# Kernel optimization log

Hardware: AMD Instinct MI355X
Metric: run time of the kernel (lower is better)

The kernel has to match this reference:

```python
import jax, jax.numpy as jnp
import numpy as np

NUM_HEADS = 8
ALPHA = 4.0
BN_EPS = 1e-5


def _dwconv(x, w, pad):
    # x: [B, C, H, W], w: [C, 1, kh, kw] depthwise (groups == C)
    return jax.lax.conv_general_dilated(
        x, w, window_strides=(1, 1), padding=[(pad, pad), (pad, pad)],
        dimension_numbers=('NCHW', 'OIHW', 'NCHW'),
        feature_group_count=x.shape[1])


def _forward(x, qg_w, kv_w, proj_w, proj_b, dwc_w, dwc_b, power_p, scale_p,
             enh_w, bn_gamma, bn_beta, enhance_weight, pos_enc):
    B, N, C = x.shape
    H = W = int(round(N ** 0.5))
    h = NUM_HEADS
    d = C // h

    # qg linear (no bias): [B, N, 2C] -> q, g
    qg = jnp.einsum('bnc,oc->bno', x, qg_w)
    q, g = qg[..., :C], qg[..., C:]

    # SpatialFilterEnhancer on q: depthwise 3x3 conv + BN(train) + ReLU
    qi = q.transpose(0, 2, 1).reshape(B, C, H, W)
    qe = _dwconv(qi, enh_w, pad=1)
    m = qe.mean(axis=(0, 2, 3), keepdims=True)
    var = qe.var(axis=(0, 2, 3), keepdims=True)
    qe = (qe - m) * jax.lax.rsqrt(var + BN_EPS)
    qe = qe * bn_gamma[None, :, None, None] + bn_beta[None, :, None, None]
    qe = jax.nn.relu(qe)
    q_enh = qe.reshape(B, C, N).transpose(0, 2, 1)
    q = q + enhance_weight * q_enh

    # kv linear (sr_ratio == 1 path)
    kv = jnp.einsum('bnc,oc->bno', x, kv_w)
    k, v = kv[..., :C], kv[..., C:]
    k = k + pos_enc  # learned positional encoding, shape [1, N, C]
    n = k.shape[1]

    scale = jax.nn.softplus(scale_p)              # [1, 1, C]
    power = 1.0 + ALPHA * jax.nn.sigmoid(power_p)  # [1, h, 1, d]
    q = q / scale
    k = k / scale

    # split heads: [B, h, N, d]
    q = q.reshape(B, N, h, d).transpose(0, 2, 1, 3)
    k = k.reshape(B, n, h, d).transpose(0, 2, 1, 3)
    v = v.reshape(B, n, h, d).transpose(0, 2, 1, 3)

    # power-law kernel feature maps
    q_pos = jax.nn.relu(q) ** power
    q_neg = jax.nn.relu(-q) ** power
    k_pos = jax.nn.relu(k) ** power
    k_neg = jax.nn.relu(-k) ** power
    q_sim = jnp.concatenate([q_pos, q_neg], axis=-1)   # [B, h, N, 2d]
    q_opp = jnp.concatenate([q_neg, q_pos], axis=-1)
    kf = jnp.concatenate([k_pos, k_neg], axis=-1)      # [B, h, n, 2d]
    v1, v2 = jnp.split(v, 2, axis=-1)                  # [B, h, n, d/2] each

    k_mean = kf.mean(axis=-2)  # [B, h, 2d]
    inv_n = 1.0 / n

    # sim branch
    z = 1.0 / (jnp.einsum('bhnd,bhd->bhn', q_sim, k_mean)[..., None] + 1e-6)
    kv1 = jnp.einsum('bhnd,bhne->bhde', kf, v1) * inv_n  # (n^-0.5)*(n^-0.5)
    x_sim = jnp.einsum('bhnd,bhde->bhne', q_sim, kv1) * z

    # opp branch
    z2 = 1.0 / (jnp.einsum('bhnd,bhd->bhn', q_opp, k_mean)[..., None] + 1e-6)
    kv2 = jnp.einsum('bhnd,bhne->bhde', kf, v2) * inv_n
    x_opp = jnp.einsum('bhnd,bhde->bhne', q_opp, kv2) * z2

    xa = jnp.concatenate([x_sim, x_opp], axis=-1)       # [B, h, N, d]
    xa = xa.transpose(0, 2, 1, 3).reshape(B, N, C)

    # depthwise conv positional branch on v (sr_ratio == 1 -> no interpolate)
    vimg = v.reshape(B * h, H, W, d).transpose(0, 3, 1, 2)  # [B*h, d, H, W]
    vd = _dwconv(vimg, dwc_w, pad=2) + dwc_b[None, :, None, None]
    v_out = vd.reshape(B, C, N).transpose(0, 2, 1)          # [B, N, C]

    out = (xa + v_out) * g
    out = jnp.einsum('bnc,oc->bno', out, proj_w) + proj_b
    return out


def setup_inputs() -> dict:
    key = jax.random.key(0)
    ks = jax.random.split(key, 10)
    B, N, C = 8, 3136, 512
    h = NUM_HEADS
    d = C // h
    f = lambda k, shape, s=0.02: jax.random.normal(k, shape, jnp.float32) * s
    return dict(
        x=jax.random.normal(ks[0], (B, N, C), jnp.float32),
        qg_w=f(ks[1], (2 * C, C)),
        kv_w=f(ks[2], (2 * C, C)),
        proj_w=f(ks[3], (C, C)),
        proj_b=jnp.zeros((C,), jnp.float32),
        dwc_w=f(ks[4], (d, 1, 5, 5), 0.1),
        dwc_b=jnp.zeros((d,), jnp.float32),
        power_p=f(ks[5], (1, h, 1, d), 0.1),
        scale_p=f(ks[6], (1, 1, C), 0.1),
        enh_w=f(ks[7], (C, 1, 3, 3), 0.1),
        bn_gamma=jnp.ones((C,), jnp.float32),
        bn_beta=jnp.zeros((C,), jnp.float32),
        enhance_weight=jnp.float32(0.5),
        pos_enc=f(ks[8], (1, N, C)),
    )


def reference(x, qg_w, kv_w, proj_w, proj_b, dwc_w, dwc_b, power_p, scale_p,
              enh_w, bn_gamma, bn_beta, enhance_weight, pos_enc):
    return _forward(x, qg_w, kv_w, proj_w, proj_b, dwc_w, dwc_b, power_p,
                    scale_p, enh_w, bn_gamma, bn_beta, enhance_weight, pos_enc)
```

## Files before the change

kernel.cpp:

```cpp
#include <hip/hip_runtime.h>
#include <hip/hip_bf16.h>
#include <math.h>

#define CDIM 512
#define NTOK 3136
#define BATCH 8
#define MTOT (BATCH*NTOK)
#define NHEAD 8
#define DHEAD 64
#define HW 56

typedef __attribute__((ext_vector_type(8))) short short8;
typedef __attribute__((ext_vector_type(4))) float f32x4;

__device__ __forceinline__ ushort f2bf(float f) {
    union { float f; unsigned int u; } v; v.f = f;
    unsigned int u = v.u + 0x7FFFu + ((v.u >> 16) & 1u);
    return (ushort)(u >> 16);
}
__device__ __forceinline__ float bf2f(ushort u) {
    union { unsigned int u; float f; } v; v.u = ((unsigned int)u) << 16;
    return v.f;
}

__device__ __forceinline__ void gload_lds16(const void* g, void* lds) {
    __builtin_amdgcn_global_load_lds((const __attribute__((address_space(1))) void*)g,
                                     (__attribute__((address_space(3))) void*)lds,
                                     16, 0, 0);
}

__global__ void prep_kernel(const float* __restrict__ scale_p,
                            const float* __restrict__ power_p,
                            float* __restrict__ inv_scale,
                            float* __restrict__ power) {
    int c = threadIdx.x;
    if (c < CDIM) {
        float s = log1pf(expf(scale_p[c]));
        inv_scale[c] = 1.0f / s;
        power[c] = 1.0f + 4.0f / (1.0f + expf(-power_p[c]));
    }
}

__global__ __launch_bounds__(256) void cvt_bf16_kernel(const float* __restrict__ src,
                                                       ushort* __restrict__ dst, int n4) {
    int i = blockIdx.x * 256 + threadIdx.x;
    if (i < n4) {
        float4 f = ((const float4*)src)[i];
        ushort4 o;
        o.x = f2bf(f.x); o.y = f2bf(f.y); o.z = f2bf(f.z); o.w = f2bf(f.w);
        ((ushort4*)dst)[i] = o;
    }
}

__global__ __launch_bounds__(256) void mgemm_qgkv(const ushort* __restrict__ A,
                                                  const ushort* __restrict__ Wqg,
                                                  const ushort* __restrict__ Wkv,
                                                  ushort* __restrict__ Qout,
                                                  ushort* __restrict__ Gout,
                                                  ushort* __restrict__ KFout,
                                                  ushort* __restrict__ Vout,
                                                  const float* __restrict__ pos,
                                                  const float* __restrict__ invs,
                                                  const float* __restrict__ powr) {
    __shared__ __align__(16) char smem[32768];
    ushort* At = (ushort*)smem;
    ushort* Bt = (ushort*)(smem + 16384);
    float*  Osh = (float*)smem;

    const int t = threadIdx.x;
    const int w = t >> 6, l = t & 63;
    const int wr = w >> 1, wc = w & 1;

    const int bid = blockIdx.x;
    const int idp = (bid & 7) * 392 + (bid >> 3);
    const int mb = idp >> 4, ob = idp & 15;
    const int m0 = mb * 128;
    const ushort* Bp = (ob < 8) ? (Wqg + (size_t)ob * 128 * CDIM)
                                : (Wkv + (size_t)(ob - 8) * 128 * CDIM);

    auto stage = [&](int buf, int ks) {
        const int k0 = ks * 32;
        #pragma unroll
        for (int i = 0; i < 2; ++i) {
            int f = t + i * 256;
            int r = f >> 2, ps = f & 3;
            int ls = ps ^ ((r >> 2) & 3);
            gload_lds16(A + (size_t)(m0 + r) * CDIM + k0 + ls * 8, At + buf * 4096 + f * 8);
            gload_lds16(Bp + (size_t)r * CDIM + k0 + ls * 8, Bt + buf * 4096 + f * 8);
        }
    };

    f32x4 acc[4][4] = {};
    const int psl = (l >> 4) ^ ((l >> 2) & 3);
    stage(0, 0);
    __syncthreads();
    for (int ks = 0; ks < 16; ++ks) {
        int cur = ks & 1;
        if (ks < 15) stage(cur ^ 1, ks + 1);
        short8 af[4], bfr[4];
        #pragma unroll
        for (int i = 0; i < 4; ++i) {
            int row = wr * 64 + i * 16 + (l & 15);
            af[i] = *(const short8*)&At[cur * 4096 + row * 32 + psl * 8];
            int rowb = wc * 64 + i * 16 + (l & 15);
            bfr[i] = *(const short8*)&Bt[cur * 4096 + rowb * 32 + psl * 8];
        }
        #pragma unroll
        for (int i = 0; i < 4; ++i)
            #pragma unroll
            for (int j = 0; j < 4; ++j)
                acc[i][j] = __builtin_amdgcn_mfma_f32_16x16x32_bf16(af[i], bfr[j], acc[i][j], 0, 0, 0);
        __syncthreads();
    }

    const int colbase = ob * 128;
    #pragma unroll
    for (int p = 0; p < 2; ++p) {
        if (wr == p) {
            #pragma unroll
            for (int i = 0; i < 4; ++i)
                #pragma unroll
                for (int j = 0; j < 4; ++j)
                    #pragma unroll
                    for (int rr = 0; rr < 4; ++rr) {
                        int r = i * 16 + (l >> 4) * 4 + rr;
                        int c = wc * 64 + j * 16 + (l & 15);
                        int pc = (c + ((r & 4) << 2)) & 127;
                        Osh[r * 128 + pc] = acc[i][j][rr];
                    }
        }
        __syncthreads();
        #pragma unroll
        for (int q = 0; q < 8; ++q) {
            int fi = q * 256 + t;
            int rl = fi >> 5;
            int r = p * 64 + rl;
            int c4 = (fi & 31) * 4;
            int pc = (c4 + ((rl & 4) << 2)) & 127;
            float4 v = *(float4*)&Osh[rl * 128 + pc];
            int m = m0 + r;
            if (colbase < 512) {
                ushort4 o;
                o.x = f2bf(v.x); o.y = f2bf(v.y); o.z = f2bf(v.z); o.w = f2bf(v.w);
                *(ushort4*)&Qout[(size_t)m * CDIM + colbase + c4] = o;
            } else if (colbase < 1024) {
                ushort4 o;
                o.x = f2bf(v.x); o.y = f2bf(v.y); o.z = f2bf(v.z); o.w = f2bf(v.w);
                *(ushort4*)&Gout[(size_t)m * CDIM + colbase - 512 + c4] = o;
            } else if (colbase < 1536) {
                int n = m % NTOK;
                int oc = colbase - 1024 + c4;
                float4 pv = *(const float4*)&pos[(size_t)n * CDIM + oc];
                float4 iv = *(const float4*)&invs[oc];
                float4 pw = *(const float4*)&powr[oc];
                float kx0 = (v.x + pv.x) * iv.x, kx1 = (v.y + pv.y) * iv.y;
                float kx2 = (v.z + pv.z) * iv.z, kx3 = (v.w + pv.w) * iv.w;
                float t0 = __powf(fabsf(kx0), pw.x), t1 = __powf(fabsf(kx1), pw.y);
                float t2 = __powf(fabsf(kx2), pw.z), t3 = __powf(fabsf(kx3), pw.w);
                ushort4 up, un;
                up.x = kx0 > 0.f ? f2bf(t0) : 0; un.x = kx0 < 0.f ? f2bf(t0) : 0;
                up.y = kx1 > 0.f ? f2bf(t1) : 0; un.y = kx1 < 0.f ? f2bf(t1) : 0;
                up.z = kx2 > 0.f ? f2bf(t2) : 0; un.z = kx2 < 0.f ? f2bf(t2) : 0;
                up.w = kx3 > 0.f ? f2bf(t3) : 0; un.w = kx3 < 0.f ? f2bf(t3) : 0;
                ushort* dst = KFout + (size_t)m * 1024 + ((oc >> 6) << 7) + (oc & 63);
                *(ushort4*)dst = up;
                *(ushort4*)(dst + 64) = un;
            } else {
                ushort4 o;
                o.x = f2bf(v.x); o.y = f2bf(v.y); o.z = f2bf(v.z); o.w = f2bf(v.w);
                *(ushort4*)&Vout[(size_t)m * CDIM + colbase - 1536 + c4] = o;
            }
        }
        __syncthreads();
    }
}

__global__ __launch_bounds__(256) void mgemm_proj(const ushort* __restrict__ A,
                                                  const ushort* __restrict__ W,
                                                  float* __restrict__ out,
                                                  const float* __restrict__ pb) {
    __shared__ __align__(16) char smem[32768];
    ushort* At = (ushort*)smem;
    ushort* Bt = (ushort*)(smem + 16384);
    float*  Osh = (float*)smem;

    const int t = threadIdx.x;
    const int w = t >> 6, l = t & 63;
    const int wr = w >> 1, wc = w & 1;

    const int bid = blockIdx.x;
    const int idp = (bid & 7) * 98 + (bid >> 3);
    const int mb = idp >> 2, ob = idp & 3;
    const int m0 = mb * 128;
    const ushort* Bp = W + (size_t)ob * 128 * CDIM;

    auto stage = [&](int buf, int ks) {
        const int k0 = ks * 32;
        #pragma unroll
        for (int i = 0; i < 2; ++i) {
            int f = t + i * 256;
            int r = f >> 2, ps = f & 3;
            int ls = ps ^ ((r >> 2) & 3);
            gload_lds16(A + (size_t)(m0 + r) * CDIM + k0 + ls * 8, At + buf * 4096 + f * 8);
            gload_lds16(Bp + (size_t)r * CDIM + k0 + ls * 8, Bt + buf * 4096 + f * 8);
        }
    };

    f32x4 acc[4][4] = {};
    const int psl = (l >> 4) ^ ((l >> 2) & 3);
    stage(0, 0);
    __syncthreads();
    for (int ks = 0; ks < 16; ++ks) {
        int cur = ks & 1;
        if (ks < 15) stage(cur ^ 1, ks + 1);
        short8 af[4], bfr[4];
        #pragma unroll
        for (int i = 0; i < 4; ++i) {
            int row = wr * 64 + i * 16 + (l & 15);
            af[i] = *(const short8*)&At[cur * 4096 + row * 32 + psl * 8];
            int rowb = wc * 64 + i * 16 + (l & 15);
            bfr[i] = *(const short8*)&Bt[cur * 4096 + rowb * 32 + psl * 8];
        }
        #pragma unroll
        for (int i = 0; i < 4; ++i)
            #pragma unroll
            for (int j = 0; j < 4; ++j)
                acc[i][j] = __builtin_amdgcn_mfma_f32_16x16x32_bf16(af[i], bfr[j], acc[i][j], 0, 0, 0);
        __syncthreads();
    }

    const int colbase = ob * 128;
    #pragma unroll
    for (int p = 0; p < 2; ++p) {
        if (wr == p) {
            #pragma unroll
            for (int i = 0; i < 4; ++i)
                #pragma unroll
                for (int j = 0; j < 4; ++j)
                    #pragma unroll
                    for (int rr = 0; rr < 4; ++rr) {
                        int r = i * 16 + (l >> 4) * 4 + rr;
                        int c = wc * 64 + j * 16 + (l & 15);
                        int pc = (c + ((r & 4) << 2)) & 127;
                        Osh[r * 128 + pc] = acc[i][j][rr];
                    }
        }
        __syncthreads();
        #pragma unroll
        for (int q = 0; q < 8; ++q) {
            int fi = q * 256 + t;
            int rl = fi >> 5;
            int r = p * 64 + rl;
            int c4 = (fi & 31) * 4;
            int pc = (c4 + ((rl & 4) << 2)) & 127;
            float4 v = *(float4*)&Osh[rl * 128 + pc];
            float4 b4 = *(const float4*)&pb[colbase + c4];
            v.x += b4.x; v.y += b4.y; v.z += b4.z; v.w += b4.w;
            *(float4*)&out[(size_t)(m0 + r) * CDIM + colbase + c4] = v;
        }
        __syncthreads();
    }
}

__global__ __launch_bounds__(256) void conv3s_kernel(const ushort* __restrict__ Qbf,
                                                     const float* __restrict__ enh_w,
                                                     ushort* __restrict__ QEbf,
                                                     float* __restrict__ ssum,
                                                     float* __restrict__ ssq) {
    const int t = threadIdx.x;
    const int c0 = t * 2;
    const int xpos = blockIdx.x;
    const int byc = blockIdx.y;
    const int b = byc >> 2, yc = byc & 3;
    const int y0 = yc * 14;

    float wgt[9][2];
    #pragma unroll
    for (int tap = 0; tap < 9; ++tap) {
        wgt[tap][0] = enh_w[c0 * 9 + tap];
        wgt[tap][1] = enh_w[(c0 + 1) * 9 + tap];
    }
    const size_t base = (size_t)b * NTOK * CDIM + c0;

    float2 win[3][3];
    auto ldrow = [&](int yy, float2* dst) {
        #pragma unroll
        for (int dx = 0; dx < 3; ++dx) {
            int xx = xpos + dx - 1;
            bool ok = (yy >= 0 && yy < HW && xx >= 0 && xx < HW);
            if (ok) {
                ushort2 uv = *(const ushort2*)(Qbf + base + ((size_t)(yy * HW + xx) << 9));
                dst[dx] = make_float2(bf2f(uv.x), bf2f(uv.y));
            } else {
                dst[dx] = make_float2(0.f, 0.f);
            }
        }
    };
    ldrow(y0 - 1, win[0]);
    ldrow(y0,     win[1]);

    float s1a = 0.f, s2a = 0.f, s1b = 0.f, s2b = 0.f;
    #pragma unroll
    for (int i = 0; i < 14; ++i) {
        int y = y0 + i;
        ldrow(y + 1, win[(i + 2) % 3]);
        float a0 = 0.f, a1 = 0.f;
        #pragma unroll
        for (int dy = 0; dy < 3; ++dy) {
            float2* row = win[(i + dy) % 3];
            #pragma unroll
            for (int dx = 0; dx < 3; ++dx) {
                a0 = fmaf(row[dx].x, wgt[dy * 3 + dx][0], a0);
                a1 = fmaf(row[dx].y, wgt[dy * 3 + dx][1], a1);
            }
        }
        ushort2 o; o.x = f2bf(a0); o.y = f2bf(a1);
        *(ushort2*)(QEbf + base + ((size_t)(y * HW + xpos) << 9)) = o;
        s1a += a0; s2a += a0 * a0;
        s1b += a1; s2b += a1 * a1;
    }
    atomicAdd(&ssum[c0], s1a);     atomicAdd(&ssq[c0], s2a);
    atomicAdd(&ssum[c0 + 1], s1b); atomicAdd(&ssq[c0 + 1], s2b);
}

__global__ void bnprep_kernel(const float* __restrict__ ssum, const float* __restrict__ ssq,
                              const float* __restrict__ bn_g, const float* __restrict__ bn_b,
                              float* __restrict__ achan, float* __restrict__ bchan) {
    int c = threadIdx.x;
    if (c < CDIM) {
        const float invM = 1.0f / (float)MTOT;
        float mean = ssum[c] * invM;
        float var  = ssq[c] * invM - mean * mean;
        float a = bn_g[c] * rsqrtf(var + 1e-5f);
        achan[c] = a;
        bchan[c] = bn_b[c] - mean * a;
    }
}

__global__ __launch_bounds__(256) void kvred4_kernel(const ushort* __restrict__ KF,
                                                     const ushort* __restrict__ Vbf,
                                                     float* __restrict__ PKV) {
    const int bh = blockIdx.x, chunk = blockIdx.y;
    const int b = bh >> 3, head = bh & 7;
    const int t = threadIdx.x;
    const int w = t >> 6, l = t & 63;
    const int lr = l & 15;
    const int ns = (l >> 4) * 8;

    const int nbase = b * NTOK + chunk * 448;
    const ushort* kf0 = KF  + ((size_t)(nbase + ns)) * 1024 + head * 128 + (w * 32 + lr);
    const ushort* vb0 = Vbf + ((size_t)(nbase + ns)) * 512  + head * 64  + lr;

    short8 ones;
    #pragma unroll
    for (int j = 0; j < 8; ++j) ones[j] = (lr == 0) ? (short)0x3F80 : (short)0;

    f32x4 acc[2][5] = {};
    for (int tile = 0; tile < 14; ++tile) {
        union { uint u[4]; short8 s; } ua[2], ub[4];
        #pragma unroll
        for (int i = 0; i < 2; ++i) {
            #pragma unroll
            for (int j = 0; j < 4; ++j) {
                uint lo = kf0[i * 16 + (size_t)(2 * j) * 1024];
                uint hi = kf0[i * 16 + (size_t)(2 * j + 1) * 1024];
                ua[i].u[j] = lo | (hi << 16);
            }
        }
        #pragma unroll
        for (int j5 = 0; j5 < 4; ++j5) {
            #pragma unroll
            for (int j = 0; j < 4; ++j) {
                uint lo = vb0[j5 * 16 + (size_t)(2 * j) * 512];
                uint hi = vb0[j5 * 16 + (size_t)(2 * j + 1) * 512];
                ub[j5].u[j] = lo | (hi << 16);
            }
        }
        #pragma unroll
        for (int i = 0; i < 2; ++i) {
            #pragma unroll
            for (int j5 = 0; j5 < 4; ++j5)
                acc[i][j5] = __builtin_amdgcn_mfma_f32_16x16x32_bf16(ua[i].s, ub[j5].s, acc[i][j5], 0, 0, 0);
            acc[i][4] = __builtin_amdgcn_mfma_f32_16x16x32_bf16(ua[i].s, ones, acc[i][4], 0, 0, 0);
        }
        kf0 += (size_t)32 * 1024;
        vb0 += (size_t)32 * 512;
    }
    size_t base = ((size_t)(chunk * 64 + bh)) * 8320;
    #pragma unroll
    for (int i = 0; i < 2; ++i) {
        int d0 = w * 32 + i * 16 + (l >> 4) * 4;
        #pragma unroll
        for (int j = 0; j < 5; ++j) {
            int e = j * 16 + lr;
            if (j < 4 || e == 64)
                *(f32x4*)(PKV + base + (size_t)e * 128 + d0) = acc[i][j];
        }
    }
}

__global__ __launch_bounds__(256) void kvreduce2_kernel(const float* __restrict__ PKV,
                                                        ushort* __restrict__ kvTbf) {
    int gid = blockIdx.x * 256 + threadIdx.x;
    const float inv_n = 1.0f / (float)NTOK;
    int bh = gid / 10240;
    int r  = gid - bh * 10240;
    int row = r >> 7, dcol = r & 127;
    int dlog = (((dcol >> 3) ^ (row & 7)) << 3) | (dcol & 7);
    float s = 0.f;
    if (row < 64) {
        int dsel = (row >= 32) ? (dlog ^ 64) : dlog;
        #pragma unroll
        for (int c = 0; c < 7; ++c) s += PKV[(size_t)c * 532480 + (size_t)bh * 8320 + row * 128 + dsel];
    } else if (row < 66) {
        int dsel = (row == 65) ? (dlog ^ 64) : dlog;
        #pragma unroll
        for (int c = 0; c < 7; ++c) s += PKV[(size_t)c * 532480 + (size_t)bh * 8320 + 64 * 128 + dsel];
    }
    kvTbf[gid] = (row < 66) ? f2bf(s * inv_n) : (ushort)0;
}

__global__ __launch_bounds__(256) void attn_mfma_kernel(const ushort* __restrict__ Qbf,
                                                        const ushort* __restrict__ QEbf,
                                                        const ushort* __restrict__ kvTbf,
                                                        const float* __restrict__ power,
                                                        const float* __restrict__ achan,
                                                        const float* __restrict__ bchan,
                                                        const float* __restrict__ invs,
                                                        const float* __restrict__ ewp,
                                                        ushort* __restrict__ ATTbf) {
    __shared__ ushort QF[64 * 128];
    __shared__ ushort BT[80 * 128];
    const int bh = blockIdx.x, tb = blockIdx.y;
    const int b = bh >> 3, head = bh & 7;
    const int t = threadIdx.x;
    const int w = t >> 6, l = t & 63;

    #pragma unroll
    for (int i = 0; i < 5; ++i) {
        int f = i * 256 + t;
        gload_lds16(kvTbf + (size_t)bh * 10240 + f * 8, BT + f * 8);
    }

    const int c = l, hc = head * 64 + c;
    const float p = power[hc];
    const float ac = achan[hc], bc = bchan[hc], iv = invs[hc], ew = ewp[0];
    #pragma unroll
    for (int i = 0; i < 16; ++i) {
        int tok = i * 4 + w;
        size_t off = ((size_t)(b * NTOK + tb * 64 + tok)) * CDIM + hc;
        float q = bf2f(Qbf[off]);
        float qe = bf2f(QEbf[off]);
        q = (q + ew * fmaxf(fmaf(ac, qe, bc), 0.f)) * iv;
        float ax = fabsf(q);
        float tp = ax > 0.f ? __powf(ax, p) : 0.f;
        float qp = q > 0.f ? tp : 0.f;
        float qn = q < 0.f ? tp : 0.f;
        int sw = tok & 7;
        QF[tok * 128 + (((c >> 3) ^ sw) * 8) + (c & 7)]       = f2bf(qp);
        QF[tok * 128 + ((((c >> 3) + 8) ^ sw) * 8) + (c & 7)] = f2bf(qn);
    }
    __syncthreads();

    f32x4 acc[5] = {};
    #pragma unroll
    for (int kk = 0; kk < 4; ++kk) {
        int sbase = kk * 4 + (l >> 4);
        int rowa = w * 16 + (l & 15);
        short8 af = *(const short8*)&QF[rowa * 128 + ((sbase ^ (rowa & 7)) * 8)];
        #pragma unroll
        for (int j = 0; j < 5; ++j) {
            int rowb = j * 16 + (l & 15);
            short8 bf = *(const short8*)&BT[rowb * 128 + ((sbase ^ (rowb & 7)) * 8)];
            acc[j] = __builtin_amdgcn_mfma_f32_16x16x32_bf16(af, bf, acc[j], 0, 0, 0);
        }
    }
    __syncthreads();

    ushort* Oout = QF;
    #pragma unroll
    for (int rr = 0; rr < 4; ++rr) {
        float ssim = __shfl(acc[4][rr], (l & 48));
        float sopp = __shfl(acc[4][rr], (l & 48) + 1);
        float zs = 1.f / (ssim + 1e-6f);
        float zo = 1.f / (sopp + 1e-6f);
        int tokl = w * 16 + (l >> 4) * 4 + rr;
        #pragma unroll
        for (int j = 0; j < 4; ++j) {
            int e = j * 16 + (l & 15);
            Oout[tokl * 64 + e] = f2bf(acc[j][rr] * (j < 2 ? zs : zo));
        }
    }
    __syncthreads();

    #pragma unroll
    for (int i = 0; i < 2; ++i) {
        int idx = i * 256 + t;
        int tokl = idx >> 3, ch = (idx & 7) * 8;
        short8 vv = *(short8*)&Oout[tokl * 64 + ch];
        *(short8*)&ATTbf[((size_t)(b * NTOK + tb * 64 + tokl)) * CDIM + head * 64 + ch] = vv;
    }
}

__global__ __launch_bounds__(256) void voutg2_kernel(const ushort* __restrict__ Vbf,
                                                     const ushort* __restrict__ ATTbf,
                                                     const ushort* __restrict__ Gbf,
                                                     const float* __restrict__ dwc_w,
                                                     const float* __restrict__ dwc_b,
                                                     ushort* __restrict__ PRE) {
    const int t = threadIdx.x;
    const int c0 = t * 2;
    const int xpos = blockIdx.x;
    const int byc = blockIdx.y;
    const int b = byc >> 2, yc = byc & 3;
    const int y0 = yc * 14;
    const int dch = c0 & 63;

    float wgt[25][2];
    #pragma unroll
    for (int tap = 0; tap < 25; ++tap) {
        wgt[tap][0] = dwc_w[dch * 25 + tap];
        wgt[tap][1] = dwc_w[(dch + 1) * 25 + tap];
    }
    const float bias0 = dwc_b[dch], bias1 = dwc_b[dch + 1];
    const size_t base = (size_t)b * NTOK * CDIM + c0;

    float2 win[5][5];
    auto ldrow = [&](int yy, float2* dst) {
        #pragma unroll
        for (int dx = 0; dx < 5; ++dx) {
            int xx = xpos + dx - 2;
            bool ok = (yy >= 0 && yy < HW && xx >= 0 && xx < HW);
            if (ok) {
                ushort2 uv = *(const ushort2*)(Vbf + base + ((size_t)(yy * HW + xx) << 9));
                dst[dx] = make_float2(bf2f(uv.x), bf2f(uv.y));
            } else {
                dst[dx] = make_float2(0.f, 0.f);
            }
        }
    };
    ldrow(y0 - 2, win[0]);
    ldrow(y0 - 1, win[1]);
    ldrow(y0,     win[2]);
    ldrow(y0 + 1, win[3]);

    #pragma unroll
    for (int i = 0; i < 14; ++i) {
        int y = y0 + i;
        ldrow(y + 2, win[(i + 4) % 5]);
        float a0 = bias0, a1 = bias1;
        #pragma unroll
        for (int dy = 0; dy < 5; ++dy) {
            float2* row = win[(i + dy) % 5];
            #pragma unroll
            for (int dx = 0; dx < 5; ++dx) {
                a0 = fmaf(row[dx].x, wgt[dy * 5 + dx][0], a0);
                a1 = fmaf(row[dx].y, wgt[dy * 5 + dx][1], a1);
            }
        }
        size_t oidx = base + ((size_t)(y * HW + xpos) << 9);
        ushort2 au = *(const ushort2*)(ATTbf + oidx);
        ushort2 gu = *(const ushort2*)(Gbf + oidx);
        ushort2 o;
        o.x = f2bf((bf2f(au.x) + a0) * bf2f(gu.x));
        o.y = f2bf((bf2f(au.y) + a1) * bf2f(gu.y));
        *(ushort2*)(PRE + oidx) = o;
    }
}

extern "C" void kernel_launch(void* const* d_in, const int* in_sizes, int n_in,
                              void* d_out, int out_size, void* d_ws, size_t ws_size,
                              hipStream_t stream) {
    const float* x      = (const float*)d_in[0];
    const float* qg_w   = (const float*)d_in[1];
    const float* kv_w   = (const float*)d_in[2];
    const float* proj_w = (const float*)d_in[3];
    const float* proj_b = (const float*)d_in[4];
    const float* dwc_w  = (const float*)d_in[5];
    const float* dwc_b  = (const float*)d_in[6];
    const float* power_p= (const float*)d_in[7];
    const float* scale_p= (const float*)d_in[8];
    const float* enh_w  = (const float*)d_in[9];
    const float* bn_g   = (const float*)d_in[10];
    const float* bn_b   = (const float*)d_in[11];
    const float* ew_p   = (const float*)d_in[12];
    const float* pos    = (const float*)d_in[13];

    const size_t NELEM = (size_t)MTOT * CDIM;
    float* ws    = (float*)d_ws;
    ushort* Qbf  = (ushort*)ws;
    ushort* Gbf  = (ushort*)(ws + NELEM);
    float*  PKV  = ws + NELEM + NELEM / 2;
    ushort* KFbf = (ushort*)(ws + 2 * NELEM);
    ushort* PREbf= (ushort*)(ws + 2 * NELEM);
    ushort* Vbf  = (ushort*)(ws + 3 * NELEM);
    ushort* ATTbf= (ushort*)(ws + 3 * NELEM + NELEM / 2);
    ushort* Xbf  = (ushort*)(ws + 4 * NELEM);
    ushort* QEbf = (ushort*)(ws + 4 * NELEM);
    float* SMALL = ws + 5 * NELEM;
    float* ssum  = SMALL;
    float* ssq   = SMALL + 512;
    ushort* kvTbf= (ushort*)(SMALL + 9216);
    float* invs  = SMALL + 533504;
    float* powr  = SMALL + 534016;
    float* achan = SMALL + 534528;
    float* bchan = SMALL + 535040;
    ushort* Wqg  = (ushort*)(SMALL + 535552);
    ushort* Wkv  = (ushort*)(SMALL + 797696);
    ushort* Wproj= (ushort*)(SMALL + 1059840);

    hipMemsetAsync(SMALL, 0, (size_t)1024 * sizeof(float), stream);

    prep_kernel<<<1, 512, 0, stream>>>(scale_p, power_p, invs, powr);

    cvt_bf16_kernel<<<12544, 256, 0, stream>>>(x, Xbf, 3211264);
    cvt_bf16_kernel<<<512, 256, 0, stream>>>(qg_w, Wqg, 131072);
    cvt_bf16_kernel<<<512, 256, 0, stream>>>(kv_w, Wkv, 131072);
    cvt_bf16_kernel<<<256, 256, 0, stream>>>(proj_w, Wproj, 65536);

    mgemm_qgkv<<<3136, 256, 0, stream>>>(Xbf, Wqg, Wkv, Qbf, Gbf, KFbf, Vbf, pos, invs, powr);

    dim3 cgrid(56, 32);
    conv3s_kernel<<<cgrid, 256, 0, stream>>>(Qbf, enh_w, QEbf, ssum, ssq);
    bnprep_kernel<<<1, 512, 0, stream>>>(ssum, ssq, bn_g, bn_b, achan, bchan);

    kvred4_kernel<<<dim3(64, 7), 256, 0, stream>>>(KFbf, Vbf, PKV);
    kvreduce2_kernel<<<2560, 256, 0, stream>>>(PKV, kvTbf);

    attn_mfma_kernel<<<dim3(64, 49), 256, 0, stream>>>(Qbf, QEbf, kvTbf, powr,
                                                       achan, bchan, invs, ew_p, ATTbf);

    voutg2_kernel<<<cgrid, 256, 0, stream>>>(Vbf, ATTbf, Gbf, dwc_w, dwc_b, PREbf);

    mgemm_proj<<<784, 256, 0, stream>>>(PREbf, Wproj, (float*)d_out, proj_b);
}
```

Before: 506.5 us.

## Double GEMM K-tile to 64 with XOR-swizzled LDS and single-pass epilogue

Both MFMA GEMM kernels (qg/kv projection and output projection) now stage 64-wide K slices instead of 32, halving the number of main-loop iterations and barriers. The LDS layout uses a new 8-way XOR swizzle to avoid bank conflicts. The epilogue writes the whole 128x128 fp32 tile to shared memory in one pass instead of two, which drops the extra barriers. Shared memory per block doubles to 64KB, which may lower occupancy.

```diff
diff --git a/kernel.cpp b/kernel.cpp
--- a/kernel.cpp
+++ b/kernel.cpp
@@ -62,14 +62,16 @@
                                                   const float* __restrict__ pos,
                                                   const float* __restrict__ invs,
                                                   const float* __restrict__ powr) {
-    __shared__ __align__(16) char smem[32768];
+    __shared__ __align__(16) char smem[65536];
     ushort* At = (ushort*)smem;
-    ushort* Bt = (ushort*)(smem + 16384);
+    ushort* Bt = (ushort*)(smem + 32768);
     float*  Osh = (float*)smem;
 
     const int t = threadIdx.x;
     const int w = t >> 6, l = t & 63;
     const int wr = w >> 1, wc = w & 1;
+    const int r8 = l >> 3, sl = l & 7;
+    const int ss = sl ^ r8;
 
     const int bid = blockIdx.x;
     const int idp = (bid & 7) * 392 + (bid >> 3);
@@ -79,99 +81,93 @@
                                 : (Wkv + (size_t)(ob - 8) * 128 * CDIM);
 
     auto stage = [&](int buf, int ks) {
-        const int k0 = ks * 32;
-        #pragma unroll
-        for (int i = 0; i < 2; ++i) {
-            int f = t + i * 256;
-            int r = f >> 2, ps = f & 3;
-            int ls = ps ^ ((r >> 2) & 3);
-            gload_lds16(A + (size_t)(m0 + r) * CDIM + k0 + ls * 8, At + buf * 4096 + f * 8);
-            gload_lds16(Bp + (size_t)r * CDIM + k0 + ls * 8, Bt + buf * 4096 + f * 8);
+        const int k0 = ks * 64;
+        #pragma unroll
+        for (int c = 0; c < 4; ++c) {
+            int rc = (w * 4 + c) * 8 + r8;
+            gload_lds16(A + (size_t)(m0 + rc) * CDIM + k0 + ss * 8, At + buf * 8192 + (w * 4 + c) * 512);
+            gload_lds16(Bp + (size_t)rc * CDIM + k0 + ss * 8, Bt + buf * 8192 + (w * 4 + c) * 512);
         }
     };
 
     f32x4 acc[4][4] = {};
-    const int psl = (l >> 4) ^ ((l >> 2) & 3);
     stage(0, 0);
     __syncthreads();
-    for (int ks = 0; ks < 16; ++ks) {
+    for (int ks = 0; ks < 8; ++ks) {
         int cur = ks & 1;
-        if (ks < 15) stage(cur ^ 1, ks + 1);
-        short8 af[4], bfr[4];
-        #pragma unroll
-        for (int i = 0; i < 4; ++i) {
-            int row = wr * 64 + i * 16 + (l & 15);
-            af[i] = *(const short8*)&At[cur * 4096 + row * 32 + psl * 8];
-            int rowb = wc * 64 + i * 16 + (l & 15);
-            bfr[i] = *(const short8*)&Bt[cur * 4096 + rowb * 32 + psl * 8];
-        }
-        #pragma unroll
-        for (int i = 0; i < 4; ++i)
-            #pragma unroll
-            for (int j = 0; j < 4; ++j)
-                acc[i][j] = __builtin_amdgcn_mfma_f32_16x16x32_bf16(af[i], bfr[j], acc[i][j], 0, 0, 0);
-        __syncthreads();
-    }
-
-    const int colbase = ob * 128;
-    #pragma unroll
-    for (int p = 0; p < 2; ++p) {
-        if (wr == p) {
+        if (ks < 7) stage(cur ^ 1, ks + 1);
+        #pragma unroll
+        for (int kk = 0; kk < 2; ++kk) {
+            short8 af[4], bfr[4];
+            const int sbase = kk * 4 + (l >> 4);
+            #pragma unroll
+            for (int i = 0; i < 4; ++i) {
+                int row = wr * 64 + i * 16 + (l & 15);
+                af[i] = *(const short8*)&At[cur * 8192 + row * 64 + ((sbase ^ (row & 7)) * 8)];
+                int rowb = wc * 64 + i * 16 + (l & 15);
+                bfr[i] = *(const short8*)&Bt[cur * 8192 + rowb * 64 + ((sbase ^ (rowb & 7)) * 8)];
+            }
             #pragma unroll
             for (int i = 0; i < 4; ++i)
                 #pragma unroll
                 for (int j = 0; j < 4; ++j)
-                    #pragma unroll
-                    for (int rr = 0; rr < 4; ++rr) {
-                        int r = i * 16 + (l >> 4) * 4 + rr;
-                        int c = wc * 64 + j * 16 + (l & 15);
-                        int pc = (c + ((r & 4) << 2)) & 127;
-                        Osh[r * 128 + pc] = acc[i][j][rr];
-                    }
+                    acc[i][j] = __builtin_amdgcn_mfma_f32_16x16x32_bf16(af[i], bfr[j], acc[i][j], 0, 0, 0);
         }
         __syncthreads();
-        #pragma unroll
-        for (int q = 0; q < 8; ++q) {
-            int fi = q * 256 + t;
-            int rl = fi >> 5;
-            int r = p * 64 + rl;
-            int c4 = (fi & 31) * 4;
-            int pc = (c4 + ((rl & 4) << 2)) & 127;
-            float4 v = *(float4*)&Osh[rl * 128 + pc];
-            int m = m0 + r;
-            if (colbase < 512) {
-                ushort4 o;
-                o.x = f2bf(v.x); o.y = f2bf(v.y); o.z = f2bf(v.z); o.w = f2bf(v.w);
-                *(ushort4*)&Qout[(size_t)m * CDIM + colbase + c4] = o;
-            } else if (colbase < 1024) {
-                ushort4 o;
-                o.x = f2bf(v.x); o.y = f2bf(v.y); o.z = f2bf(v.z); o.w = f2bf(v.w);
-                *(ushort4*)&Gout[(size_t)m * CDIM + colbase - 512 + c4] = o;
-            } else if (colbase < 1536) {
-                int n = m % NTOK;
-                int oc = colbase - 1024 + c4;
-                float4 pv = *(const float4*)&pos[(size_t)n * CDIM + oc];
-                float4 iv = *(const float4*)&invs[oc];
-                float4 pw = *(const float4*)&powr[oc];
-                float kx0 = (v.x + pv.x) * iv.x, kx1 = (v.y + pv.y) * iv.y;
-                float kx2 = (v.z + pv.z) * iv.z, kx3 = (v.w + pv.w) * iv.w;
-                float t0 = __powf(fabsf(kx0), pw.x), t1 = __powf(fabsf(kx1), pw.y);
-                float t2 = __powf(fabsf(kx2), pw.z), t3 = __powf(fabsf(kx3), pw.w);
-                ushort4 up, un;
-                up.x = kx0 > 0.f ? f2bf(t0) : 0; un.x = kx0 < 0.f ? f2bf(t0) : 0;
-                up.y = kx1 > 0.f ? f2bf(t1) : 0; un.y = kx1 < 0.f ? f2bf(t1) : 0;
-                up.z = kx2 > 0.f ? f2bf(t2) : 0; un.z = kx2 < 0.f ? f2bf(t2) : 0;
-                up.w = kx3 > 0.f ? f2bf(t3) : 0; un.w = kx3 < 0.f ? f2bf(t3) : 0;
-                ushort* dst = KFout + (size_t)m * 1024 + ((oc >> 6) << 7) + (oc & 63);
-                *(ushort4*)dst = up;
-                *(ushort4*)(dst + 64) = un;
-            } else {
-                ushort4 o;
-                o.x = f2bf(v.x); o.y = f2bf(v.y); o.z = f2bf(v.z); o.w = f2bf(v.w);
-                *(ushort4*)&Vout[(size_t)m * CDIM + colbase - 1536 + c4] = o;
-            }
-        }
-        __syncthreads();
+    }
+
+    #pragma unroll
+    for (int i = 0; i < 4; ++i)
+        #pragma unroll
+        for (int j = 0; j < 4; ++j)
+            #pragma unroll
+            for (int rr = 0; rr < 4; ++rr) {
+                int row = wr * 64 + i * 16 + (l >> 4) * 4 + rr;
+                int col = wc * 64 + j * 16 + (l & 15);
+                int pc = col ^ (((row >> 2) & 1) << 4);
+                Osh[row * 128 + pc] = acc[i][j][rr];
+            }
+    __syncthreads();
+
+    const int colbase = ob * 128;
+    #pragma unroll
+    for (int q = 0; q < 16; ++q) {
+        int fi = q * 256 + t;
+        int r = fi >> 5, c4 = (fi & 31) * 4;
+        int pc4 = c4 ^ (((r >> 2) & 1) << 4);
+        float4 v = *(float4*)&Osh[r * 128 + pc4];
+        int m = m0 + r;
+        if (colbase < 512) {
+            ushort4 o;
+            o.x = f2bf(v.x); o.y = f2bf(v.y); o.z = f2bf(v.z); o.w = f2bf(v.w);
+            *(ushort4*)&Qout[(size_t)m * CDIM + colbase + c4] = o;
+        } else if (colbase < 1024) {
+            ushort4 o;
+            o.x = f2bf(v.x); o.y = f2bf(v.y); o.z = f2bf(v.z); o.w = f2bf(v.w);
+            *(ushort4*)&Gout[(size_t)m * CDIM + colbase - 512 + c4] = o;
+        } else if (colbase < 1536) {
+            int n = m % NTOK;
+            int oc = colbase - 1024 + c4;
+            float4 pv = *(const float4*)&pos[(size_t)n * CDIM + oc];
+            float4 iv = *(const float4*)&invs[oc];
+            float4 pw = *(const float4*)&powr[oc];
+            float kx0 = (v.x + pv.x) * iv.x, kx1 = (v.y + pv.y) * iv.y;
+            float kx2 = (v.z + pv.z) * iv.z, kx3 = (v.w + pv.w) * iv.w;
+            float t0 = __powf(fabsf(kx0), pw.x), t1 = __powf(fabsf(kx1), pw.y);
+            float t2 = __powf(fabsf(kx2), pw.z), t3 = __powf(fabsf(kx3), pw.w);
+            ushort4 up, un;
+            up.x = kx0 > 0.f ? f2bf(t0) : 0; un.x = kx0 < 0.f ? f2bf(t0) : 0;
+            up.y = kx1 > 0.f ? f2bf(t1) : 0; un.y = kx1 < 0.f ? f2bf(t1) : 0;
+            up.z = kx2 > 0.f ? f2bf(t2) : 0; un.z = kx2 < 0.f ? f2bf(t2) : 0;
+            up.w = kx3 > 0.f ? f2bf(t3) : 0; un.w = kx3 < 0.f ? f2bf(t3) : 0;
+            ushort* dst = KFout + (size_t)m * 1024 + ((oc >> 6) << 7) + (oc & 63);
+            *(ushort4*)dst = up;
+            *(ushort4*)(dst + 64) = un;
+        } else {
+            ushort4 o;
+            o.x = f2bf(v.x); o.y = f2bf(v.y); o.z = f2bf(v.z); o.w = f2bf(v.w);
+            *(ushort4*)&Vout[(size_t)m * CDIM + colbase - 1536 + c4] = o;
+        }
     }
 }
 
@@ -179,14 +175,16 @@
                                                   const ushort* __restrict__ W,
                                                   float* __restrict__ out,
                                                   const float* __restrict__ pb) {
-    __shared__ __align__(16) char smem[32768];
+    __shared__ __align__(16) char smem[65536];
     ushort* At = (ushort*)smem;
-    ushort* Bt = (ushort*)(smem + 16384);
+    ushort* Bt = (ushort*)(smem + 32768);
     float*  Osh = (float*)smem;
 
     const int t = threadIdx.x;
     const int w = t >> 6, l = t & 63;
     const int wr = w >> 1, wc = w & 1;
+    const int r8 = l >> 3, sl = l & 7;
+    const int ss = sl ^ r8;
 
     const int bid = blockIdx.x;
     const int idp = (bid & 7) * 98 + (bid >> 3);
@@ -195,70 +193,64 @@
     const ushort* Bp = W + (size_t)ob * 128 * CDIM;
 
     auto stage = [&](int buf, int ks) {
-        const int k0 = ks * 32;
-        #pragma unroll
-        for (int i = 0; i < 2; ++i) {
-            int f = t + i * 256;
-            int r = f >> 2, ps = f & 3;
-            int ls = ps ^ ((r >> 2) & 3);
-            gload_lds16(A + (size_t)(m0 + r) * CDIM + k0 + ls * 8, At + buf * 4096 + f * 8);
-            gload_lds16(Bp + (size_t)r * CDIM + k0 + ls * 8, Bt + buf * 4096 + f * 8);
+        const int k0 = ks * 64;
+        #pragma unroll
+        for (int c = 0; c < 4; ++c) {
+            int rc = (w * 4 + c) * 8 + r8;
+            gload_lds16(A + (size_t)(m0 + rc) * CDIM + k0 + ss * 8, At + buf * 8192 + (w * 4 + c) * 512);
+            gload_lds16(Bp + (size_t)rc * CDIM + k0 + ss * 8, Bt + buf * 8192 + (w * 4 + c) * 512);
         }
     };
 
     f32x4 acc[4][4] = {};
-    const int psl = (l >> 4) ^ ((l >> 2) & 3);
     stage(0, 0);
     __syncthreads();
-    for (int ks = 0; ks < 16; ++ks) {
+    for (int ks = 0; ks < 8; ++ks) {
         int cur = ks & 1;
-        if (ks < 15) stage(cur ^ 1, ks + 1);
-        short8 af[4], bfr[4];
-        #pragma unroll
-        for (int i = 0; i < 4; ++i) {
-            int row = wr * 64 + i * 16 + (l & 15);
-            af[i] = *(const short8*)&At[cur * 4096 + row * 32 + psl * 8];
-            int rowb = wc * 64 + i * 16 + (l & 15);
-            bfr[i] = *(const short8*)&Bt[cur * 4096 + rowb * 32 + psl * 8];
-        }
-        #pragma unroll
-        for (int i = 0; i < 4; ++i)
-            #pragma unroll
-            for (int j = 0; j < 4; ++j)
-                acc[i][j] = __builtin_amdgcn_mfma_f32_16x16x32_bf16(af[i], bfr[j], acc[i][j], 0, 0, 0);
-        __syncthreads();
-    }
-
-    const int colbase = ob * 128;
-    #pragma unroll
-    for (int p = 0; p < 2; ++p) {
-        if (wr == p) {
+        if (ks < 7) stage(cur ^ 1, ks + 1);
+        #pragma unroll
+        for (int kk = 0; kk < 2; ++kk) {
+            short8 af[4], bfr[4];
+            const int sbase = kk * 4 + (l >> 4);
+            #pragma unroll
+            for (int i = 0; i < 4; ++i) {
+                int row = wr * 64 + i * 16 + (l & 15);
+                af[i] = *(const short8*)&At[cur * 8192 + row * 64 + ((sbase ^ (row & 7)) * 8)];
+                int rowb = wc * 64 + i * 16 + (l & 15);
+                bfr[i] = *(const short8*)&Bt[cur * 8192 + rowb * 64 + ((sbase ^ (rowb & 7)) * 8)];
+            }
             #pragma unroll
             for (int i = 0; i < 4; ++i)
                 #pragma unroll
                 for (int j = 0; j < 4; ++j)
-                    #pragma unroll
-                    for (int rr = 0; rr < 4; ++rr) {
-                        int r = i * 16 + (l >> 4) * 4 + rr;
-                        int c = wc * 64 + j * 16 + (l & 15);
-                        int pc = (c + ((r & 4) << 2)) & 127;
-                        Osh[r * 128 + pc] = acc[i][j][rr];
-                    }
+                    acc[i][j] = __builtin_amdgcn_mfma_f32_16x16x32_bf16(af[i], bfr[j], acc[i][j], 0, 0, 0);
         }
         __syncthreads();
-        #pragma unroll
-        for (int q = 0; q < 8; ++q) {
-            int fi = q * 256 + t;
-            int rl = fi >> 5;
-            int r = p * 64 + rl;
-            int c4 = (fi & 31) * 4;
-            int pc = (c4 + ((rl & 4) << 2)) & 127;
-            float4 v = *(float4*)&Osh[rl * 128 + pc];
-            float4 b4 = *(const float4*)&pb[colbase + c4];
-            v.x += b4.x; v.y += b4.y; v.z += b4.z; v.w += b4.w;
-            *(float4*)&out[(size_t)(m0 + r) * CDIM + colbase + c4] = v;
-        }
-        __syncthreads();
+    }
+
+    #pragma unroll
+    for (int i = 0; i < 4; ++i)
+        #pragma unroll
+        for (int j = 0; j < 4; ++j)
+            #pragma unroll
+            for (int rr = 0; rr < 4; ++rr) {
+                int row = wr * 64 + i * 16 + (l >> 4) * 4 + rr;
+                int col = wc * 64 + j * 16 + (l & 15);
+                int pc = col ^ (((row >> 2) & 1) << 4);
+                Osh[row * 128 + pc] = acc[i][j][rr];
+            }
+    __syncthreads();
+
+    const int colbase = ob * 128;
+    #pragma unroll
+    for (int q = 0; q < 16; ++q) {
+        int fi = q * 256 + t;
+        int r = fi >> 5, c4 = (fi & 31) * 4;
+        int pc4 = c4 ^ (((r >> 2) & 1) << 4);
+        float4 v = *(float4*)&Osh[r * 128 + pc4];
+        float4 b4 = *(const float4*)&pb[colbase + c4];
+        v.x += b4.x; v.y += b4.y; v.z += b4.z; v.w += b4.w;
+        *(float4*)&out[(size_t)(m0 + r) * CDIM + colbase + c4] = v;
     }
 }
 
```

Measured after the change: 502.2 us, median of 2. About the same (-0.8%).
